# Kernel optimization log

Measured on AMD Instinct MI355X. Metric: run time of the kernel, lower is better.

Reference implementation:

```python
import jax, jax.numpy as jnp
import numpy as np

B, P, C, T, V, H, A = 256, 620, 512, 32, 140, 256, 256


def setup_inputs() -> dict:
    key = jax.random.key(0)
    ks = jax.random.split(key, 8)
    s = lambda k, shape, sc: (jax.random.normal(k, shape, jnp.float32) * sc)
    return {
        "img_features": jax.random.normal(ks[0], (B, P, C), jnp.float32),
        "targets": jax.random.normal(ks[1], (B, T, V), jnp.float32),
        "Ic_w": s(ks[2], (A, C), 0.02), "Ic_b": jnp.zeros((A,), jnp.float32),
        "Hc_w": s(ks[3], (A, H), 0.02), "Hc_b": jnp.zeros((A,), jnp.float32),
        "W_ih": s(ks[4], (4 * H, V + A), 0.02), "W_hh": s(ks[5], (4 * H, H), 0.02),
        "b_ih": jnp.zeros((4 * H,), jnp.float32), "b_hh": jnp.zeros((4 * H,), jnp.float32),
        "Cd_w": s(ks[6], (V, H), 0.02), "Cd_b": jnp.zeros((V,), jnp.float32),
    }


def reference(img_features, targets, Ic_w, Ic_b, Hc_w, Hc_b,
              W_ih, W_hh, b_ih, b_hh, Cd_w, Cd_b):
    # Project image features once: attn_img = Ic(img_features)  [B,P,A]
    attn_img = jnp.einsum('bpc,ac->bpa', img_features, Ic_w) + Ic_b
    scale = 1.0 / jnp.sqrt(jnp.float32(A))
    h0 = jnp.zeros((B, H), jnp.float32)
    c0 = jnp.zeros((B, H), jnp.float32)
    x0 = targets[:, 0, :]  # <start> token logits/one-hot, fed as first rnn input

    def step(carry, _):
        h, c, x = carry
        # attn_hidden = Hc(hidden): [B,A]
        q = h @ Hc_w.T + Hc_b
        # scaled dot-product attention over pixels (keys=values=attn_img)
        w = jax.nn.softmax(jnp.einsum('ba,bpa->bp', q, attn_img) * scale, axis=-1)
        ctx = jnp.einsum('bp,bpa->ba', w, attn_img)  # [B,A]
        # single-step LSTM (PyTorch gate order: i, f, g, o)
        inp = jnp.concatenate([x, ctx], axis=-1)  # [B, V+A]
        gates = inp @ W_ih.T + b_ih + h @ W_hh.T + b_hh
        i, f, g, o = jnp.split(gates, 4, axis=-1)
        c2 = jax.nn.sigmoid(f) * c + jax.nn.sigmoid(i) * jnp.tanh(g)
        h2 = jax.nn.sigmoid(o) * jnp.tanh(c2)
        out = h2 @ Cd_w.T + Cd_b  # [B,V] vocab logits
        # eval path: next rnn_input is the predicted logits
        return (h2, c2, out), out

    _, outs = jax.lax.scan(step, (h0, c0, x0), None, length=T)
    return jnp.transpose(outs, (1, 0, 2))  # [B,T,V]
```

## Files before the change

kernel.cpp:

```cpp
#include <hip/hip_runtime.h>
#include <stdint.h>

#define B_ 256
#define P_ 620
#define C_ 512
#define T_ 32
#define V_ 140
#define H_ 256
#define A_ 256
#define KC 672
#define LOG2E 1.4426950408889634f

typedef unsigned short u16;
typedef __attribute__((ext_vector_type(8))) short bf16x8;
typedef __attribute__((ext_vector_type(4))) float f32x4;

__device__ __forceinline__ float bf2f(u16 u) {
  union { unsigned int i; float f; } v; v.i = ((unsigned int)u) << 16; return v.f;
}
__device__ __forceinline__ float bfu_lo(unsigned int u) {
  union { unsigned int i; float f; } v; v.i = u << 16; return v.f;
}
__device__ __forceinline__ float bfu_hi(unsigned int u) {
  union { unsigned int i; float f; } v; v.i = u & 0xffff0000u; return v.f;
}
__device__ __forceinline__ u16 f2bf(float f) {
  union { float f; unsigned int i; } v; v.f = f;
  unsigned int x = v.i;
  return (u16)((x + 0x7fffu + ((x >> 16) & 1u)) >> 16);
}
__device__ __forceinline__ float sigf(float x) {
  return 1.f / (1.f + __builtin_exp2f(-x * LOG2E));
}
__device__ __forceinline__ float tanhfast(float x) {
  return 1.f - 2.f / (__builtin_exp2f(2.f * LOG2E * x) + 1.f);
}
__device__ __forceinline__ float ld_any(const void* p, size_t idx, int f32) {
  return f32 ? ((const float*)p)[idx] : bf2f(((const u16*)p)[idx]);
}
__device__ __forceinline__ bf16x8 ld8_any(const void* base, size_t off, int f32) {
  if (f32) {
    const float4* p = (const float4*)((const float*)base + off);
    float4 x = p[0], y = p[1];
    bf16x8 r;
    r[0] = (short)f2bf(x.x); r[1] = (short)f2bf(x.y);
    r[2] = (short)f2bf(x.z); r[3] = (short)f2bf(x.w);
    r[4] = (short)f2bf(y.x); r[5] = (short)f2bf(y.y);
    r[6] = (short)f2bf(y.z); r[7] = (short)f2bf(y.w);
    return r;
  }
  return *(const bf16x8*)((const u16*)base + off);
}
__device__ __forceinline__ float dot8(uint4 u, float4 iA, float4 iB) {
  return bfu_lo(u.x) * iA.x + bfu_hi(u.x) * iA.y
       + bfu_lo(u.y) * iA.z + bfu_hi(u.y) * iA.w
       + bfu_lo(u.z) * iB.x + bfu_hi(u.z) * iB.y
       + bfu_lo(u.w) * iB.z + bfu_hi(u.w) * iB.w;
}

__global__ void k_detect(const unsigned int* __restrict__ img, int* __restrict__ flag) {
  __shared__ int mx[256];
  unsigned int u = img[threadIdx.x];
  mx[threadIdx.x] = (int)((u >> 7) & 0xffu);
  __syncthreads();
  if (threadIdx.x == 0) {
    int m = 0;
    #pragma unroll 16
    for (int i = 0; i < 256; i++) m = (mx[i] > m) ? mx[i] : m;
    *flag = (m >= 0x90) ? 1 : 0;
  }
}

__global__ void k_init(const void* __restrict__ W_ih, const void* __restrict__ W_hh,
                       const void* __restrict__ b_ih, const void* __restrict__ b_hh,
                       const void* __restrict__ Hc_w, const void* __restrict__ Hc_b,
                       const void* __restrict__ Cd_w, const void* __restrict__ Cd_b,
                       u16* __restrict__ W2, float* __restrict__ bias_cat,
                       unsigned int* __restrict__ Hc_p, float* __restrict__ hcb_f,
                       unsigned int* __restrict__ Cd_p, float* __restrict__ cdb_f,
                       const int* __restrict__ flag) {
  const int f32 = *flag;
  const int tid = blockIdx.x * blockDim.x + threadIdx.x;
  const int nthr = gridDim.x * blockDim.x;
  for (int idx = tid; idx < 1024 * KC; idx += nthr) {
    int jq = idx / KC, k = idx - jq * KC;
    int j = jq >> 2, q = jq & 3, n = q * H_ + j;
    u16 v = 0;
    if (k < 396) v = f2bf(ld_any(W_ih, (size_t)n * 396 + k, f32));
    else if (k < 652) v = f2bf(ld_any(W_hh, (size_t)n * H_ + (k - 396), f32));
    const int kk = k >> 3, e = k & 7, blk = jq >> 8, r = jq & 255;
    W2[((size_t)(kk * 4 + blk) * 256 + r) * 8 + e] = v;
  }
  for (int n = tid; n < 1024; n += nthr) {
    int j = n >> 2, q = n & 3, on = q * H_ + j;
    bias_cat[n] = ld_any(b_ih, on, f32) + ld_any(b_hh, on, f32);
  }
  for (int idx = tid; idx < 128 * 256; idx += nthr) {
    int j2 = idx >> 8, n = idx & 255;
    u16 lo = f2bf(ld_any(Hc_w, (size_t)n * H_ + 2 * j2, f32));
    u16 hi = f2bf(ld_any(Hc_w, (size_t)n * H_ + 2 * j2 + 1, f32));
    Hc_p[idx] = (unsigned int)lo | ((unsigned int)hi << 16);
  }
  for (int idx = tid; idx < 128 * 140; idx += nthr) {
    int j2 = idx / 140, v = idx - j2 * 140;
    u16 lo = f2bf(ld_any(Cd_w, (size_t)v * H_ + 2 * j2, f32));
    u16 hi = f2bf(ld_any(Cd_w, (size_t)v * H_ + 2 * j2 + 1, f32));
    Cd_p[idx] = (unsigned int)lo | ((unsigned int)hi << 16);
  }
  for (int n = tid; n < A_; n += nthr) hcb_f[n] = ld_any(Hc_b, n, f32);
  for (int n = tid; n < V_; n += nthr) cdb_f[n] = ld_any(Cd_b, n, f32);
}

__global__ __launch_bounds__(256) void k_proj(const void* __restrict__ img,
                                              const void* __restrict__ Ic_w,
                                              const void* __restrict__ Ic_b,
                                              u16* __restrict__ attn_img,
                                              const int* __restrict__ flag) {
  __shared__ __align__(16) short As[128 * 32];
  __shared__ __align__(16) short Bs[128 * 32];
  const int f32 = *flag;
  const int tid = threadIdx.x;
  const int lane = tid & 63, w = tid >> 6;
  const int wg = blockIdx.x;
  const int m0 = ((wg & 7) + (wg >> 4) * 8) * 128;
  const int n0 = ((wg >> 3) & 1) * 128;
  f32x4 acc[4][4] = {};
  const int wm = w & 1, wn = w >> 1;
  const int fr = lane & 15, fq = lane >> 4;
  const int srow = tid >> 2, scol = (tid & 3) * 8;
  for (int kt = 0; kt < C_; kt += 32) {
    bf16x8 a0 = ld8_any(img, (size_t)(m0 + srow) * C_ + kt + scol, f32);
    bf16x8 a1 = ld8_any(img, (size_t)(m0 + srow + 64) * C_ + kt + scol, f32);
    bf16x8 b0 = ld8_any(Ic_w, (size_t)(n0 + srow) * C_ + kt + scol, f32);
    bf16x8 b1 = ld8_any(Ic_w, (size_t)(n0 + srow + 64) * C_ + kt + scol, f32);
    __syncthreads();
    *(bf16x8*)(As + tid * 8) = a0;
    *(bf16x8*)(As + (tid + 256) * 8) = a1;
    *(bf16x8*)(Bs + tid * 8) = b0;
    *(bf16x8*)(Bs + (tid + 256) * 8) = b1;
    __syncthreads();
    bf16x8 af[4], bfr[4];
    #pragma unroll
    for (int i = 0; i < 4; i++)
      af[i] = *(const bf16x8*)(As + (wm * 64 + i * 16 + fr) * 32 + fq * 8);
    #pragma unroll
    for (int j = 0; j < 4; j++)
      bfr[j] = *(const bf16x8*)(Bs + (wn * 64 + j * 16 + fr) * 32 + fq * 8);
    #pragma unroll
    for (int i = 0; i < 4; i++)
      #pragma unroll
      for (int j = 0; j < 4; j++)
        acc[i][j] = __builtin_amdgcn_mfma_f32_16x16x32_bf16(af[i], bfr[j], acc[i][j], 0, 0, 0);
  }
  #pragma unroll
  for (int i = 0; i < 4; i++) {
    #pragma unroll
    for (int j = 0; j < 4; j++) {
      const int col = n0 + wn * 64 + j * 16 + fr;
      const float bias = ld_any(Ic_b, col, f32);
      #pragma unroll
      for (int rr = 0; rr < 4; rr++) {
        const int row = m0 + wm * 64 + i * 16 + fq * 4 + rr;
        attn_img[(size_t)row * A_ + col] = f2bf(acc[i][j][rr] + bias);
      }
    }
  }
}

__global__ __launch_bounds__(512, 2) void k_seq(
    const unsigned int* __restrict__ Hc_p, const float* __restrict__ hcb_f,
    const unsigned int* __restrict__ Cd_p, const float* __restrict__ cdb_f,
    const u16* __restrict__ W2, const float* __restrict__ bias_cat,
    const u16* __restrict__ attn_img, const void* __restrict__ targets,
    void* __restrict__ d_out, const int* __restrict__ flag) {
  __shared__ float h_s[H_];
  __shared__ float q_s[A_];
  __shared__ __align__(16) float inp_s[KC];
  __shared__ __align__(16) float ctx_s[4][A_];
  __shared__ float red_l[4];
  __shared__ __align__(16) float gpart[1024];
  const int f32 = *flag;
  const int b = blockIdx.x;
  const int tid = threadIdx.x;
  const int lane = tid & 63, w = tid >> 6;
  const uint4* wb = (const uint4*)W2;

  if (tid < H_) h_s[tid] = 0.f;
  for (int i = tid; i < KC; i += 512) inp_s[i] = 0.f;
  if (tid < V_) inp_s[tid] = ld_any(targets, (size_t)b * T_ * V_ + tid, f32);
  float c_reg = 0.f;
  float bias_b0 = 0.f, bias_b1 = 0.f, bias_b2 = 0.f, bias_b3 = 0.f;
  if (tid >= 256) {
    const int r = tid - 256;
    bias_b0 = bias_cat[r];       bias_b1 = bias_cat[256 + r];
    bias_b2 = bias_cat[512 + r]; bias_b3 = bias_cat[768 + r];
  }
  const float sc = 0.0625f * LOG2E;
  __syncthreads();

  for (int t = 0; t < T_; t++) {
    if (tid < A_) {
      float acc = hcb_f[tid];
      #pragma unroll 8
      for (int j2 = 0; j2 < H_ / 2; j2++) {
        const unsigned int u = Hc_p[j2 * 256 + tid];
        acc += bfu_lo(u) * h_s[2 * j2] + bfu_hi(u) * h_s[2 * j2 + 1];
      }
      q_s[tid] = acc;
    } else if (t > 0 && tid < A_ + V_) {
      const int v = tid - A_;
      float acc = cdb_f[v];
      #pragma unroll 8
      for (int j2 = 0; j2 < H_ / 2; j2++) {
        const unsigned int u = Cd_p[j2 * 140 + v];
        acc += bfu_lo(u) * h_s[2 * j2] + bfu_hi(u) * h_s[2 * j2 + 1];
      }
      const size_t oo = (size_t)b * T_ * V_ + (size_t)(t - 1) * V_ + v;
      if (f32) ((float*)d_out)[oo] = acc;
      else ((u16*)d_out)[oo] = f2bf(acc);
      inp_s[v] = acc;
    }
    __syncthreads();

    if (w < 4) {
      const int l16 = lane & 15, g = lane >> 4;
      float qr[16];
      #pragma unroll
      for (int e = 0; e < 8; e++) {
        qr[e] = q_s[l16 * 8 + e];
        qr[8 + e] = q_s[128 + l16 * 8 + e];
      }
      const uint4* ap = (const uint4*)(attn_img + (size_t)b * P_ * A_);
      const int pbase = w * 4 + g;
      uint4 cu0 = ap[(size_t)pbase * 32 + l16];
      uint4 cu1 = ap[(size_t)pbase * 32 + 16 + l16];
      uint4 nu0 = ap[(size_t)(pbase + 16) * 32 + l16];
      uint4 nu1 = ap[(size_t)(pbase + 16) * 32 + 16 + l16];
      float l_acc = 0.f;
      float cx[16] = {};
      for (int it = 0; it < 39; it++) {
        int pf = pbase + (it + 2) * 16;
        pf = (pf < P_) ? pf : (P_ - 1);
        const uint4 fu0 = ap[(size_t)pf * 32 + l16];
        const uint4 fu1 = ap[(size_t)pf * 32 + 16 + l16];
        const int p = pbase + it * 16;
        float v[16];
        v[0] = bfu_lo(cu0.x); v[1] = bfu_hi(cu0.x);
        v[2] = bfu_lo(cu0.y); v[3] = bfu_hi(cu0.y);
        v[4] = bfu_lo(cu0.z); v[5] = bfu_hi(cu0.z);
        v[6] = bfu_lo(cu0.w); v[7] = bfu_hi(cu0.w);
        v[8] = bfu_lo(cu1.x); v[9] = bfu_hi(cu1.x);
        v[10] = bfu_lo(cu1.y); v[11] = bfu_hi(cu1.y);
        v[12] = bfu_lo(cu1.z); v[13] = bfu_hi(cu1.z);
        v[14] = bfu_lo(cu1.w); v[15] = bfu_hi(cu1.w);
        float s0 = qr[0] * v[0] + qr[1] * v[1] + qr[2] * v[2] + qr[3] * v[3];
        float s1 = qr[4] * v[4] + qr[5] * v[5] + qr[6] * v[6] + qr[7] * v[7];
        float s2 = qr[8] * v[8] + qr[9] * v[9] + qr[10] * v[10] + qr[11] * v[11];
        float s3 = qr[12] * v[12] + qr[13] * v[13] + qr[14] * v[14] + qr[15] * v[15];
        float s = (s0 + s1) + (s2 + s3);
        s += __shfl_xor(s, 1); s += __shfl_xor(s, 2);
        s += __shfl_xor(s, 4); s += __shfl_xor(s, 8);
        const float sl = (p < P_) ? s * sc : -3.0e38f;
        const float es = __builtin_exp2f(sl - 16.f);
        l_acc += es;
        #pragma unroll
        for (int k = 0; k < 16; k++) cx[k] += es * v[k];
        cu0 = nu0; cu1 = nu1; nu0 = fu0; nu1 = fu1;
      }
      #pragma unroll
      for (int k = 0; k < 16; k++) {
        cx[k] += __shfl_xor(cx[k], 16);
        cx[k] += __shfl_xor(cx[k], 32);
      }
      l_acc += __shfl_xor(l_acc, 16);
      l_acc += __shfl_xor(l_acc, 32);
      if (g == 0) {
        #pragma unroll
        for (int e = 0; e < 8; e++) {
          ctx_s[w][l16 * 8 + e] = cx[e];
          ctx_s[w][128 + l16 * 8 + e] = cx[8 + e];
        }
        if (l16 == 0) red_l[w] = l_acc;
      }
    } else {
      const int r = tid - 256;
      float g0 = bias_b0, g1 = bias_b1, g2 = bias_b2, g3 = bias_b3;
      int kk = 0;
      uint4 a0 = wb[(0 * 4 + 0) * 256 + r];
      uint4 a1 = wb[(0 * 4 + 1) * 256 + r];
      uint4 a2 = wb[(0 * 4 + 2) * 256 + r];
      uint4 a3 = wb[(0 * 4 + 3) * 256 + r];
      #pragma unroll 3
      for (int i = 0; i < 51; i++) {
        const int ni = (i + 1 < 51) ? i + 1 : 50;
        const int nk = ni + ((ni >= 17) ? 33 : 0);
        const uint4 b0v = wb[(nk * 4 + 0) * 256 + r];
        const uint4 b1v = wb[(nk * 4 + 1) * 256 + r];
        const uint4 b2v = wb[(nk * 4 + 2) * 256 + r];
        const uint4 b3v = wb[(nk * 4 + 3) * 256 + r];
        const float4 iA = *(const float4*)(inp_s + kk * 8);
        const float4 iB = *(const float4*)(inp_s + kk * 8 + 4);
        g0 += dot8(a0, iA, iB); g1 += dot8(a1, iA, iB);
        g2 += dot8(a2, iA, iB); g3 += dot8(a3, iA, iB);
        a0 = b0v; a1 = b1v; a2 = b2v; a3 = b3v; kk = nk;
      }
      gpart[r] = g0; gpart[256 + r] = g1;
      gpart[512 + r] = g2; gpart[768 + r] = g3;
    }
    __syncthreads();

    if (tid < A_) {
      const float l = red_l[0] + red_l[1] + red_l[2] + red_l[3];
      const float cv = ctx_s[0][tid] + ctx_s[1][tid] + ctx_s[2][tid] + ctx_s[3][tid];
      inp_s[V_ + tid] = cv / l;
    }
    __syncthreads();

    {
      float g0 = gpart[tid], g1 = gpart[tid + 512];
      const int blo = tid >> 8, rr = tid & 255;
      uint4 a0 = wb[(17 * 4 + blo) * 256 + rr];
      uint4 a1 = wb[(17 * 4 + 2 + blo) * 256 + rr];
      #pragma unroll 4
      for (int kk = 17; kk < 50; kk++) {
        const int nk = (kk + 1 < 50) ? kk + 1 : 49;
        const uint4 b0v = wb[(nk * 4 + blo) * 256 + rr];
        const uint4 b1v = wb[(nk * 4 + 2 + blo) * 256 + rr];
        const float4 iA = *(const float4*)(inp_s + kk * 8);
        const float4 iB = *(const float4*)(inp_s + kk * 8 + 4);
        g0 += dot8(a0, iA, iB);
        g1 += dot8(a1, iA, iB);
        a0 = b0v; a1 = b1v;
      }
      gpart[tid] = g0; gpart[tid + 512] = g1;
    }
    __syncthreads();

    if (tid < H_) {
      const float4 g4 = *(const float4*)(gpart + 4 * tid);
      const float is = sigf(g4.x), fs = sigf(g4.y);
      const float gt = tanhfast(g4.z), os = sigf(g4.w);
      const float cn = fs * c_reg + is * gt;
      const float h2 = os * tanhfast(cn);
      c_reg = cn;
      h_s[tid] = h2;
      inp_s[V_ + A_ + tid] = h2;
    }
    __syncthreads();
  }

  if (tid < V_) {
    float acc = cdb_f[tid];
    #pragma unroll 8
    for (int j2 = 0; j2 < H_ / 2; j2++) {
      const unsigned int u = Cd_p[j2 * 140 + tid];
      acc += bfu_lo(u) * h_s[2 * j2] + bfu_hi(u) * h_s[2 * j2 + 1];
    }
    const size_t oo = (size_t)b * T_ * V_ + (size_t)(T_ - 1) * V_ + tid;
    if (f32) ((float*)d_out)[oo] = acc;
    else ((u16*)d_out)[oo] = f2bf(acc);
  }
}

extern "C" void kernel_launch(void* const* d_in, const int* in_sizes, int n_in,
                              void* d_out, int out_size, void* d_ws, size_t ws_size,
                              hipStream_t stream) {
  (void)in_sizes; (void)n_in; (void)out_size; (void)ws_size;
  const void* img  = d_in[0];
  const void* tgt  = d_in[1];
  const void* Ic_w = d_in[2];
  const void* Ic_b = d_in[3];
  const void* Hc_w = d_in[4];
  const void* Hc_b = d_in[5];
  const void* W_ih = d_in[6];
  const void* W_hh = d_in[7];
  const void* b_ih = d_in[8];
  const void* b_hh = d_in[9];
  const void* Cd_w = d_in[10];
  const void* Cd_b = d_in[11];

  char* ws = (char*)d_ws;
  size_t off = 0;
  auto alloc = [&](size_t bytes) -> void* {
    void* p = ws + off;
    off += (bytes + 255) & ~(size_t)255;
    return p;
  };
  u16*   attn_img = (u16*)alloc((size_t)B_ * P_ * A_ * 2);
  u16*   W2       = (u16*)alloc((size_t)1024 * KC * 2);
  float* bias_cat = (float*)alloc(1024 * 4);
  unsigned int* Hc_p = (unsigned int*)alloc((size_t)128 * 256 * 4);
  float* hcb_f    = (float*)alloc(A_ * 4);
  unsigned int* Cd_p = (unsigned int*)alloc((size_t)128 * 140 * 4);
  float* cdb_f    = (float*)alloc(V_ * 4);
  int*   flag     = (int*)alloc(256);

  k_detect<<<dim3(1), dim3(256), 0, stream>>>((const unsigned int*)img, flag);
  k_init<<<dim3(512), dim3(256), 0, stream>>>(W_ih, W_hh, b_ih, b_hh,
                                              Hc_w, Hc_b, Cd_w, Cd_b,
                                              W2, bias_cat,
                                              Hc_p, hcb_f, Cd_p, cdb_f, flag);
  k_proj<<<dim3(2480), dim3(256), 0, stream>>>(img, Ic_w, Ic_b, attn_img, flag);
  k_seq<<<dim3(B_), dim3(512), 0, stream>>>(Hc_p, hcb_f, Cd_p, cdb_f,
                                            W2, bias_cat, attn_img, tgt, d_out, flag);
}
```

Baseline: 1.730 ms.

## Keep per-batch attention keys resident in registers and LDS across timesteps

Each block now loads its batch's attention-image rows once before the time loop, keeping the first 64 pixels in shared memory and the rest in per-thread registers, instead of streaming them from global memory at every one of the 32 steps. The attention work is spread across all 8 waves, and every wave also runs the gate matvec with a 2-gate-per-thread split, replacing the earlier split where four waves did attention and four did gates. The W2 repack in init is rewritten so writes are linear. Holding 36 uint4 values per thread raises register pressure considerably, which may cause spills or lower occupancy under launch_bounds(512,2).

Result: slower. 3.631 ms (+109.9%).

```diff
diff --git a/kernel.cpp b/kernel.cpp
--- a/kernel.cpp
+++ b/kernel.cpp
@@ -10,6 +10,8 @@
 #define A_ 256
 #define KC 672
 #define LOG2E 1.4426950408889634f
+#define NLDSP 64
+#define NREGIT 18
 
 typedef unsigned short u16;
 typedef __attribute__((ext_vector_type(8))) short bf16x8;
@@ -83,13 +85,13 @@
   const int tid = blockIdx.x * blockDim.x + threadIdx.x;
   const int nthr = gridDim.x * blockDim.x;
   for (int idx = tid; idx < 1024 * KC; idx += nthr) {
-    int jq = idx / KC, k = idx - jq * KC;
-    int j = jq >> 2, q = jq & 3, n = q * H_ + j;
+    const int e = idx & 7, rr = (idx >> 3) & 255, blk = (idx >> 11) & 3, kk = idx >> 13;
+    const int k = kk * 8 + e, jq = blk * 256 + rr;
+    const int j = jq >> 2, q = jq & 3, n = q * H_ + j;
     u16 v = 0;
     if (k < 396) v = f2bf(ld_any(W_ih, (size_t)n * 396 + k, f32));
     else if (k < 652) v = f2bf(ld_any(W_hh, (size_t)n * H_ + (k - 396), f32));
-    const int kk = k >> 3, e = k & 7, blk = jq >> 8, r = jq & 255;
-    W2[((size_t)(kk * 4 + blk) * 256 + r) * 8 + e] = v;
+    W2[idx] = v;
   }
   for (int n = tid; n < 1024; n += nthr) {
     int j = n >> 2, q = n & 3, on = q * H_ + j;
@@ -167,34 +169,68 @@
   }
 }
 
+#define ACCUM(U0, U1, VALID) do {                                              \
+  const float v0 = bfu_lo((U0).x), v1 = bfu_hi((U0).x);                        \
+  const float v2 = bfu_lo((U0).y), v3 = bfu_hi((U0).y);                        \
+  const float v4 = bfu_lo((U0).z), v5 = bfu_hi((U0).z);                        \
+  const float v6 = bfu_lo((U0).w), v7 = bfu_hi((U0).w);                        \
+  const float v8 = bfu_lo((U1).x), v9 = bfu_hi((U1).x);                        \
+  const float va = bfu_lo((U1).y), vb = bfu_hi((U1).y);                        \
+  const float vc = bfu_lo((U1).z), vd = bfu_hi((U1).z);                        \
+  const float ve = bfu_lo((U1).w), vf = bfu_hi((U1).w);                        \
+  float s = qr[0]*v0 + qr[1]*v1 + qr[2]*v2 + qr[3]*v3                          \
+          + qr[4]*v4 + qr[5]*v5 + qr[6]*v6 + qr[7]*v7                          \
+          + qr[8]*v8 + qr[9]*v9 + qr[10]*va + qr[11]*vb                        \
+          + qr[12]*vc + qr[13]*vd + qr[14]*ve + qr[15]*vf;                     \
+  s += __shfl_xor(s, 1); s += __shfl_xor(s, 2);                                \
+  s += __shfl_xor(s, 4); s += __shfl_xor(s, 8);                                \
+  const float es = (VALID) ? __builtin_exp2f(s * sc - 16.f) : 0.f;             \
+  l_acc += es;                                                                 \
+  cx[0] += es*v0; cx[1] += es*v1; cx[2] += es*v2; cx[3] += es*v3;              \
+  cx[4] += es*v4; cx[5] += es*v5; cx[6] += es*v6; cx[7] += es*v7;              \
+  cx[8] += es*v8; cx[9] += es*v9; cx[10] += es*va; cx[11] += es*vb;            \
+  cx[12] += es*vc; cx[13] += es*vd; cx[14] += es*ve; cx[15] += es*vf;          \
+} while (0)
+
 __global__ __launch_bounds__(512, 2) void k_seq(
     const unsigned int* __restrict__ Hc_p, const float* __restrict__ hcb_f,
     const unsigned int* __restrict__ Cd_p, const float* __restrict__ cdb_f,
     const u16* __restrict__ W2, const float* __restrict__ bias_cat,
     const u16* __restrict__ attn_img, const void* __restrict__ targets,
     void* __restrict__ d_out, const int* __restrict__ flag) {
+  __shared__ __align__(16) uint4 attn_lds[NLDSP * 32];
   __shared__ float h_s[H_];
   __shared__ float q_s[A_];
   __shared__ __align__(16) float inp_s[KC];
-  __shared__ __align__(16) float ctx_s[4][A_];
-  __shared__ float red_l[4];
+  __shared__ __align__(16) float ctx_s[8][A_];
+  __shared__ float red_l[8];
   __shared__ __align__(16) float gpart[1024];
   const int f32 = *flag;
   const int b = blockIdx.x;
   const int tid = threadIdx.x;
   const int lane = tid & 63, w = tid >> 6;
+  const int l16 = lane & 15, g = lane >> 4;
+  const int pbase = w * 4 + g;
   const uint4* wb = (const uint4*)W2;
+  const int blk = tid >> 8, rr = tid & 255;
+
+  const uint4* ap = (const uint4*)(attn_img + (size_t)b * P_ * A_);
+  uint4 ar0[NREGIT], ar1[NREGIT];
+  #pragma unroll
+  for (int it = 0; it < NREGIT; it++) {
+    int p = NLDSP + pbase + it * 32;
+    int pc = (p < P_) ? p : (P_ - 1);
+    ar0[it] = ap[(size_t)pc * 32 + l16];
+    ar1[it] = ap[(size_t)pc * 32 + 16 + l16];
+  }
+  for (int i = tid; i < NLDSP * 32; i += 512) attn_lds[i] = ap[i];
 
   if (tid < H_) h_s[tid] = 0.f;
   for (int i = tid; i < KC; i += 512) inp_s[i] = 0.f;
   if (tid < V_) inp_s[tid] = ld_any(targets, (size_t)b * T_ * V_ + tid, f32);
   float c_reg = 0.f;
-  float bias_b0 = 0.f, bias_b1 = 0.f, bias_b2 = 0.f, bias_b3 = 0.f;
-  if (tid >= 256) {
-    const int r = tid - 256;
-    bias_b0 = bias_cat[r];       bias_b1 = bias_cat[256 + r];
-    bias_b2 = bias_cat[512 + r]; bias_b3 = bias_cat[768 + r];
-  }
+  const float bias0 = bias_cat[tid];
+  const float bias1 = bias_cat[tid + 512];
   const float sc = 0.0625f * LOG2E;
   __syncthreads();
 
@@ -222,51 +258,28 @@
     }
     __syncthreads();
 
-    if (w < 4) {
-      const int l16 = lane & 15, g = lane >> 4;
+    uint4 ga0 = wb[(0 * 4 + blk) * 256 + rr];
+    uint4 ga1 = wb[(0 * 4 + 2 + blk) * 256 + rr];
+
+    float l_acc = 0.f;
+    float cx[16] = {};
+    {
       float qr[16];
       #pragma unroll
       for (int e = 0; e < 8; e++) {
         qr[e] = q_s[l16 * 8 + e];
         qr[8 + e] = q_s[128 + l16 * 8 + e];
       }
-      const uint4* ap = (const uint4*)(attn_img + (size_t)b * P_ * A_);
-      const int pbase = w * 4 + g;
-      uint4 cu0 = ap[(size_t)pbase * 32 + l16];
-      uint4 cu1 = ap[(size_t)pbase * 32 + 16 + l16];
-      uint4 nu0 = ap[(size_t)(pbase + 16) * 32 + l16];
-      uint4 nu1 = ap[(size_t)(pbase + 16) * 32 + 16 + l16];
-      float l_acc = 0.f;
-      float cx[16] = {};
-      for (int it = 0; it < 39; it++) {
-        int pf = pbase + (it + 2) * 16;
-        pf = (pf < P_) ? pf : (P_ - 1);
-        const uint4 fu0 = ap[(size_t)pf * 32 + l16];
-        const uint4 fu1 = ap[(size_t)pf * 32 + 16 + l16];
-        const int p = pbase + it * 16;
-        float v[16];
-        v[0] = bfu_lo(cu0.x); v[1] = bfu_hi(cu0.x);
-        v[2] = bfu_lo(cu0.y); v[3] = bfu_hi(cu0.y);
-        v[4] = bfu_lo(cu0.z); v[5] = bfu_hi(cu0.z);
-        v[6] = bfu_lo(cu0.w); v[7] = bfu_hi(cu0.w);
-        v[8] = bfu_lo(cu1.x); v[9] = bfu_hi(cu1.x);
-        v[10] = bfu_lo(cu1.y); v[11] = bfu_hi(cu1.y);
-        v[12] = bfu_lo(cu1.z); v[13] = bfu_hi(cu1.z);
-        v[14] = bfu_lo(cu1.w); v[15] = bfu_hi(cu1.w);
-        float s0 = qr[0] * v[0] + qr[1] * v[1] + qr[2] * v[2] + qr[3] * v[3];
-        float s1 = qr[4] * v[4] + qr[5] * v[5] + qr[6] * v[6] + qr[7] * v[7];
-        float s2 = qr[8] * v[8] + qr[9] * v[9] + qr[10] * v[10] + qr[11] * v[11];
-        float s3 = qr[12] * v[12] + qr[13] * v[13] + qr[14] * v[14] + qr[15] * v[15];
-        float s = (s0 + s1) + (s2 + s3);
-        s += __shfl_xor(s, 1); s += __shfl_xor(s, 2);
-        s += __shfl_xor(s, 4); s += __shfl_xor(s, 8);
-        const float sl = (p < P_) ? s * sc : -3.0e38f;
-        const float es = __builtin_exp2f(sl - 16.f);
-        l_acc += es;
-        #pragma unroll
-        for (int k = 0; k < 16; k++) cx[k] += es * v[k];
-        cu0 = nu0; cu1 = nu1; nu0 = fu0; nu1 = fu1;
-      }
+      #pragma unroll
+      for (int it = 0; it < 2; it++) {
+        const int p = pbase + it * 32;
+        const uint4 u0 = attn_lds[p * 32 + l16];
+        const uint4 u1 = attn_lds[p * 32 + 16 + l16];
+        ACCUM(u0, u1, true);
+      }
+      #pragma unroll
+      for (int it = 0; it < NREGIT - 1; it++) ACCUM(ar0[it], ar1[it], true);
+      ACCUM(ar0[NREGIT - 1], ar1[NREGIT - 1], pbase < 12);
       #pragma unroll
       for (int k = 0; k < 16; k++) {
         cx[k] += __shfl_xor(cx[k], 16);
@@ -282,57 +295,51 @@
         }
         if (l16 == 0) red_l[w] = l_acc;
       }
-    } else {
-      const int r = tid - 256;
-      float g0 = bias_b0, g1 = bias_b1, g2 = bias_b2, g3 = bias_b3;
-      int kk = 0;
-      uint4 a0 = wb[(0 * 4 + 0) * 256 + r];
-      uint4 a1 = wb[(0 * 4 + 1) * 256 + r];
-      uint4 a2 = wb[(0 * 4 + 2) * 256 + r];
-      uint4 a3 = wb[(0 * 4 + 3) * 256 + r];
+    }
+
+    float g0 = bias0, g1 = bias1;
+    {
+      int ck = 0;
       #pragma unroll 3
       for (int i = 0; i < 51; i++) {
         const int ni = (i + 1 < 51) ? i + 1 : 50;
-        const int nk = ni + ((ni >= 17) ? 33 : 0);
-        const uint4 b0v = wb[(nk * 4 + 0) * 256 + r];
-        const uint4 b1v = wb[(nk * 4 + 1) * 256 + r];
-        const uint4 b2v = wb[(nk * 4 + 2) * 256 + r];
-        const uint4 b3v = wb[(nk * 4 + 3) * 256 + r];
-        const float4 iA = *(const float4*)(inp_s + kk * 8);
-        const float4 iB = *(const float4*)(inp_s + kk * 8 + 4);
-        g0 += dot8(a0, iA, iB); g1 += dot8(a1, iA, iB);
-        g2 += dot8(a2, iA, iB); g3 += dot8(a3, iA, iB);
-        a0 = b0v; a1 = b1v; a2 = b2v; a3 = b3v; kk = nk;
-      }
-      gpart[r] = g0; gpart[256 + r] = g1;
-      gpart[512 + r] = g2; gpart[768 + r] = g3;
+        const int nk = (ni < 17) ? ni : ni + 33;
+        const uint4 b0v = wb[(nk * 4 + blk) * 256 + rr];
+        const uint4 b1v = wb[(nk * 4 + 2 + blk) * 256 + rr];
+        const float4 iA = *(const float4*)(inp_s + ck * 8);
+        const float4 iB = *(const float4*)(inp_s + ck * 8 + 4);
+        g0 += dot8(ga0, iA, iB);
+        g1 += dot8(ga1, iA, iB);
+        ga0 = b0v; ga1 = b1v; ck = nk;
+      }
     }
     __syncthreads();
 
     if (tid < A_) {
-      const float l = red_l[0] + red_l[1] + red_l[2] + red_l[3];
-      const float cv = ctx_s[0][tid] + ctx_s[1][tid] + ctx_s[2][tid] + ctx_s[3][tid];
+      float l = red_l[0];
+      float cv = ctx_s[0][tid];
+      #pragma unroll
+      for (int i = 1; i < 8; i++) { l += red_l[i]; cv += ctx_s[i][tid]; }
       inp_s[V_ + tid] = cv / l;
     }
     __syncthreads();
 
     {
-      float g0 = gpart[tid], g1 = gpart[tid + 512];
-      const int blo = tid >> 8, rr = tid & 255;
-      uint4 a0 = wb[(17 * 4 + blo) * 256 + rr];
-      uint4 a1 = wb[(17 * 4 + 2 + blo) * 256 + rr];
+      uint4 a0 = wb[(17 * 4 + blk) * 256 + rr];
+      uint4 a1 = wb[(17 * 4 + 2 + blk) * 256 + rr];
       #pragma unroll 4
       for (int kk = 17; kk < 50; kk++) {
         const int nk = (kk + 1 < 50) ? kk + 1 : 49;
-        const uint4 b0v = wb[(nk * 4 + blo) * 256 + rr];
-        const uint4 b1v = wb[(nk * 4 + 2 + blo) * 256 + rr];
+        const uint4 b0v = wb[(nk * 4 + blk) * 256 + rr];
+        const uint4 b1v = wb[(nk * 4 + 2 + blk) * 256 + rr];
         const float4 iA = *(const float4*)(inp_s + kk * 8);
         const float4 iB = *(const float4*)(inp_s + kk * 8 + 4);
         g0 += dot8(a0, iA, iB);
         g1 += dot8(a1, iA, iB);
         a0 = b0v; a1 = b1v;
       }
-      gpart[tid] = g0; gpart[tid + 512] = g1;
+      gpart[tid] = g0;
+      gpart[tid + 512] = g1;
     }
     __syncthreads();
 
```
